# Kernel optimization log

Hardware: AMD Instinct MI355X
Metric: run time of the kernel (lower is better)

Reference implementation:

```python
import jax, jax.numpy as jnp
import numpy as np

H = 32  # rnn/encoder/residual hidden dim
NEG = -1e9


def gru(x, h0, Wih, Whh, bih, bhh):
    # x: (B,T,D), h0: (B,H); torch GRU gate order [r,z,n]
    xp = jnp.swapaxes(x @ Wih.T + bih, 0, 1)  # (T,B,3H)

    def step(h, xt):
        gh = h @ Whh.T + bhh
        xr, xz, xn = jnp.split(xt, 3, axis=-1)
        hr, hz, hn = jnp.split(gh, 3, axis=-1)
        r = jax.nn.sigmoid(xr + hr)
        z = jax.nn.sigmoid(xz + hz)
        n = jnp.tanh(xn + r * hn)
        h_new = (1.0 - z) * n + z * h
        return h_new, h_new

    hT, ys = jax.lax.scan(step, h0, xp)
    return jnp.swapaxes(ys, 0, 1), hT  # (B,T,H), (B,H)


def setup_inputs():
    key = jax.random.key(0)
    ks = jax.random.split(key, 30)
    B, T = 2048, 128
    def lin(k, o, i):
        return jax.random.normal(k, (o, i), jnp.float32) / np.sqrt(i)
    inp = {}
    inp['obs'] = jax.random.normal(ks[0], (B, T, 15), jnp.float32)
    inp['rnn_state'] = jax.random.normal(ks[1], (1, B, 3 * H), jnp.float32)
    inp['enc_air_W'] = lin(ks[2], H, 7); inp['enc_air_b'] = jnp.zeros((H,), jnp.float32)
    inp['enc_m_W'] = lin(ks[3], H, 4); inp['enc_m_b'] = jnp.zeros((H,), jnp.float32)
    inp['air_Wih'] = lin(ks[4], 3 * H, H); inp['air_Whh'] = lin(ks[5], 3 * H, H)
    inp['air_bih'] = jnp.zeros((3 * H,), jnp.float32); inp['air_bhh'] = jnp.zeros((3 * H,), jnp.float32)
    inp['m_Wih'] = lin(ks[6], 3 * H, H); inp['m_Whh'] = lin(ks[7], 3 * H, H)
    inp['m_bih'] = jnp.zeros((3 * H,), jnp.float32); inp['m_bhh'] = jnp.zeros((3 * H,), jnp.float32)
    inp['attn_in_w'] = lin(ks[8], 3 * H, H); inp['attn_in_b'] = jnp.zeros((3 * H,), jnp.float32)
    inp['attn_out_w'] = lin(ks[9], H, H); inp['attn_out_b'] = jnp.zeros((H,), jnp.float32)
    inp['mlp_W0'] = lin(ks[10], 256, 2 * H); inp['mlp_b0'] = jnp.zeros((256,), jnp.float32)
    inp['mlp_W1'] = lin(ks[11], 256, 256); inp['mlp_b1'] = jnp.zeros((256,), jnp.float32)
    inp['out_W'] = lin(ks[12], 1, 256); inp['out_b'] = jnp.zeros((1,), jnp.float32)
    return inp


def reference(obs, rnn_state, enc_air_W, enc_air_b, enc_m_W, enc_m_b,
              air_Wih, air_Whh, air_bih, air_bhh,
              m_Wih, m_Whh, m_bih, m_bhh,
              attn_in_w, attn_in_b, attn_out_w, attn_out_b,
              mlp_W0, mlp_b0, mlp_W1, mlp_b1, out_W, out_b):
    B, T, _ = obs.shape
    h_air0 = rnn_state[0, :, :H]                       # (B,H)
    h_m0 = rnn_state[0, :, H:].reshape(2 * B, H)       # faithful reshape (1,B,64)->(1,2B,32)

    # aircraft branch
    air_emb = obs[..., 8:] @ enc_air_W.T + enc_air_b   # (B,T,H)
    air_feat, next_h_air = gru(air_emb, h_air0, air_Wih, air_Whh, air_bih, air_bhh)

    # missile branch: concat missiles along batch dim
    m_raw = jnp.concatenate([obs[..., 0:4], obs[..., 4:8]], axis=0)  # (2B,T,4)
    m_emb = m_raw @ enc_m_W.T + enc_m_b
    m_feat, next_h_m = gru(m_emb, h_m0, m_Wih, m_Whh, m_bih, m_bhh)
    m1_feat, m2_feat = m_feat[:B], m_feat[B:]

    # inactive-missile mask from raw obs
    obs_flat = obs.reshape(-1, 15)
    inact = jnp.array([1.0, 0.0, 1.0, 0.0], jnp.float32)
    mask = jnp.stack([
        jnp.all(jnp.isclose(obs_flat[:, 0:4], inact), axis=-1),
        jnp.all(jnp.isclose(obs_flat[:, 4:8], inact), axis=-1),
    ], axis=1)                                          # (N,2) True = masked

    N = B * T
    air_flat = air_feat.reshape(N, H)
    m1_flat = m1_feat.reshape(N, H)
    m2_flat = m2_feat.reshape(N, H)

    # 2-head attention, q len 1, kv len 2
    Wq, Wk, Wv = jnp.split(attn_in_w, 3, axis=0)
    bq, bk, bv = jnp.split(attn_in_b, 3, axis=0)
    nh, hd = 2, H // 2
    qh = (air_flat @ Wq.T + bq).reshape(N, nh, hd)
    kv = jnp.stack([m1_flat, m2_flat], axis=1)          # (N,2,H)
    kh = (kv @ Wk.T + bk).reshape(N, 2, nh, hd)
    vh = (kv @ Wv.T + bv).reshape(N, 2, nh, hd)
    scores = jnp.einsum('nhd,nkhd->nhk', qh, kh) / np.sqrt(hd)
    scores = scores + jnp.where(mask[:, None, :], NEG, 0.0)
    w = jax.nn.softmax(scores, axis=-1)
    ctx = jnp.einsum('nhk,nkhd->nhd', w, vh).reshape(N, H)
    attn = ctx @ attn_out_w.T + attn_out_b
    attn = jnp.where(jnp.all(mask, axis=-1, keepdims=True), 0.0, attn)  # torch nan_to_num(all-masked)

    fusion = jnp.concatenate([air_flat, attn], axis=-1)  # (N,2H)
    h1 = jax.nn.leaky_relu(fusion @ mlp_W0.T + mlp_b0, 0.01)
    h2 = jax.nn.leaky_relu(h1 @ mlp_W1.T + mlp_b1, 0.01)
    val = h2 @ out_W.T + out_b                           # (N,1)

    next_h = jnp.concatenate([next_h_air, next_h_m.reshape(B, 2 * H)], axis=-1)[None]  # (1,B,96)
    return val, next_h
```

## Files before the change

### kernel.cpp

```cpp
#include <hip/hip_runtime.h>
#include <hip/hip_bf16.h>

#define BB 2048
#define TT 128
#define NN (BB*TT)
#define NVAL NN

#define OFF_BCA   768u
#define OFF_BCM   1632u
#define OFF_W0P   2048u
#define OFF_W1P   10240u
#define OFF_WQKV  43008u
#define OFF_WO    44544u
#define OFF_WH2A  45568u
#define OFF_WH2M  47104u
#define OFF_WC2A  48640u
#define OFF_WC2M  49024u
#define OFF_AIRF  83968u
#define OFF_MF    8472576u
#define OFF_MASK  25249792u

typedef __attribute__((ext_vector_type(8))) short short8;
typedef __attribute__((ext_vector_type(4))) float f32x4;
typedef _Float16 h2 __attribute__((ext_vector_type(2)));

__device__ __forceinline__ unsigned short f2bf(float f) {
    unsigned u = __builtin_bit_cast(unsigned, f);
    u += 0x7FFFu + ((u >> 16) & 1u);
    return (unsigned short)(u >> 16);
}
__device__ __forceinline__ unsigned f2h(float f) {
    _Float16 h = (_Float16)f;
    return (unsigned)__builtin_bit_cast(unsigned short, h);
}
__device__ __forceinline__ unsigned pkh2(float a, float b) {
    return (f2h(b) << 16) | f2h(a);
}
__device__ __forceinline__ float dot2(unsigned w, unsigned x, float acc) {
    return __builtin_amdgcn_fdot2(__builtin_bit_cast(h2, w),
                                  __builtin_bit_cast(h2, x), acc, false);
}

__global__ __launch_bounds__(256) void prep_kernel(
    const float* __restrict__ enc_air_W, const float* __restrict__ enc_air_b,
    const float* __restrict__ enc_m_W,   const float* __restrict__ enc_m_b,
    const float* __restrict__ air_Wih,   const float* __restrict__ air_bih,
    const float* __restrict__ m_Wih,     const float* __restrict__ m_bih,
    const float* __restrict__ air_Whh,   const float* __restrict__ m_Whh,
    const float* __restrict__ W0,        const float* __restrict__ W1,
    const float* __restrict__ attn_in_w, const float* __restrict__ attn_out_w,
    float* __restrict__ ws)
{
    int b = blockIdx.x, t = threadIdx.x;
    if (b == 0) {
        if (t < 96) {
            float bacc = air_bih[t];
            for (int k = 0; k < 32; k++) bacc += air_Wih[t*32+k] * enc_air_b[k];
            ws[OFF_BCA + t] = bacc;
            float bacc2 = m_bih[t];
            for (int k = 0; k < 32; k++) bacc2 += m_Wih[t*32+k] * enc_m_b[k];
            ws[OFF_BCM + t] = bacc2;
        }
    } else if (b <= 32) {
        unsigned short* w1p = (unsigned short*)(ws + OFF_W1P);
        int base = ((b-1)*256 + t);
        int lane = base & 63;
        int ctf  = base >> 6;
        int ct   = ctf & 15, s = ctf >> 4;
        int col = lane & 15, quad = lane >> 4;
        int k0 = s*32 + quad*8;
        int o  = ct*16 + col;
        #pragma unroll
        for (int j = 0; j < 8; j++)
            w1p[base*8 + j] = f2bf(W1[o*256 + k0 + j]);
    } else if (b <= 40) {
        unsigned short* w0p = (unsigned short*)(ws + OFF_W0P);
        int base = ((b-33)*256 + t);
        int lane = base & 63;
        int ctf  = base >> 6;
        int ct   = ctf & 15, s = ctf >> 4;
        int col = lane & 15, quad = lane >> 4;
        int k0 = s*32 + quad*8;
        int o  = ct*16 + col;
        #pragma unroll
        for (int j = 0; j < 8; j++)
            w0p[base*8 + j] = f2bf(W0[o*64 + k0 + j]);
    } else if (b == 41) {
        unsigned short* wqkv = (unsigned short*)(ws + OFF_WQKV);
        unsigned short* wop  = (unsigned short*)(ws + OFF_WO);
        for (int slot = t; slot < 512; slot += 256) {
            if (slot < 384) {
                int ct = slot >> 6, lane = slot & 63;
                int col = lane & 15, quad = lane >> 4;
                int o = ct*16 + col;
                #pragma unroll
                for (int j = 0; j < 8; j++)
                    wqkv[slot*8 + j] = f2bf(attn_in_w[o*32 + quad*8 + j]);
            } else {
                int s2 = slot - 384;
                int ct = s2 >> 6, lane = s2 & 63;
                int col = lane & 15, quad = lane >> 4;
                #pragma unroll
                for (int j = 0; j < 8; j++)
                    wop[s2*8 + j] = f2bf(attn_out_w[(ct*16+col)*32 + quad*8 + j]);
            }
        }
    } else if (b == 42) {
        unsigned* wa = (unsigned*)(ws + OFF_WH2A);
        unsigned* wm = (unsigned*)(ws + OFF_WH2M);
        for (int s = t; s < 3072; s += 256) {
            int s2 = (s < 1536) ? s : s - 1536;
            const float* W = (s < 1536) ? air_Whh : m_Whh;
            unsigned* dst = (s < 1536) ? wa : wm;
            int o = s2 >> 4, j = s2 & 15;
            dst[s2] = pkh2(W[o*32 + 2*j], W[o*32 + 2*j + 1]);
        }
    } else {
        unsigned* wa = (unsigned*)(ws + OFF_WC2A);
        unsigned* wm = (unsigned*)(ws + OFF_WC2M);
        for (int s = t; s < 768; s += 256) {
            int s2 = (s < 384) ? s : s - 384;
            bool is_air = (s < 384);
            unsigned* dst = is_air ? wa : wm;
            int o = s2 >> 2, j = s2 & 3;
            int ni  = is_air ? 7 : 4;
            float c0 = 0.f, c1 = 0.f;
            int i0 = 2*j, i1 = 2*j + 1;
            if (i0 < ni)
                for (int k = 0; k < 32; k++)
                    c0 += (is_air ? air_Wih[o*32+k]*enc_air_W[k*7+i0]
                                  : m_Wih[o*32+k]*enc_m_W[k*4+i0]);
            if (i1 < ni)
                for (int k = 0; k < 32; k++)
                    c1 += (is_air ? air_Wih[o*32+k]*enc_air_W[k*7+i1]
                                  : m_Wih[o*32+k]*enc_m_W[k*4+i1]);
            dst[s2] = pkh2(c0, c1);
        }
    }
}

template<int NI, int NP, bool DO_MASK>
__device__ void gru_row(const float* __restrict__ in_base,
                        const unsigned* __restrict__ wc2,
                        const float* __restrict__ bc,
                        const unsigned* __restrict__ wh2,
                        const float* __restrict__ bhh,
                        float h0,
                        float* __restrict__ feat_out,
                        float* __restrict__ hT_out,
                        float* __restrict__ mask_out,
                        int lane, int half)
{
    unsigned whr[16], whz[16], whn[16];
    #pragma unroll
    for (int j = 0; j < 16; j++) {
        whr[j] = wh2[lane*16 + j];
        whz[j] = wh2[(32+lane)*16 + j];
        whn[j] = wh2[(64+lane)*16 + j];
    }
    unsigned cr2[NP], cz2[NP], cn2[NP];
    #pragma unroll
    for (int j = 0; j < NP; j++) {
        cr2[j] = wc2[lane*4 + j];
        cz2[j] = wc2[(32+lane)*4 + j];
        cn2[j] = wc2[(64+lane)*4 + j];
    }
    const float bcr = bc[lane], bcz = bc[32+lane], bcn = bc[64+lane];
    const float bhr = bhh[lane], bhz = bhh[32+lane], bhn = bhh[64+lane];

    float h = h0;
    for (int t = 0; t < TT; t++) {
        float xin = (lane < NI) ? in_base[t*15 + lane] : 0.f;

        bool ok = true;
        if (DO_MASK) {
            bool pred = true;
            if (lane < 4) {
                const float c   = ((lane & 1) == 0) ? 1.f : 0.f;
                const float thr = ((lane & 1) == 0) ? 1.00001e-5f : 1e-8f;
                pred = fabsf(xin - c) <= thr;
            }
            unsigned long long ball = __ballot(pred);
            ok = (((ball >> (half*32)) & 0xFull) == 0xFull);
        }

        unsigned x16 = f2h(xin);
        unsigned xnb = (unsigned)__shfl_xor((int)x16, 1, 32);
        unsigned xpk = (xnb << 16) | x16;

        float ar = bcr, az = bcz, an = bcn;
        #pragma unroll
        for (int j = 0; j < NP; j++) {
            unsigned px = (unsigned)__shfl((int)xpk, 2*j, 32);
            ar = dot2(cr2[j], px, ar);
            az = dot2(cz2[j], px, az);
            an = dot2(cn2[j], px, an);
        }

        unsigned h16 = f2h(h);
        unsigned hnb = (unsigned)__shfl_xor((int)h16, 1, 32);
        unsigned hpk = (hnb << 16) | h16;

        float hr = bhr, hz = bhz, hn = bhn;
        #pragma unroll
        for (int j = 0; j < 16; j++) {
            unsigned ph = (unsigned)__shfl((int)hpk, 2*j, 32);
            hr = dot2(whr[j], ph, hr);
            hz = dot2(whz[j], ph, hz);
            hn = dot2(whn[j], ph, hn);
        }

        float r = 1.f / (1.f + __expf(-(ar + hr)));
        float z = 1.f / (1.f + __expf(-(az + hz)));
        float pre = an + r*hn;
        float e2 = __expf(2.f*pre);
        float n = 1.f - 2.f/(e2 + 1.f);
        h = n + z*(h - n);
        feat_out[t*32 + lane] = h;
        if (DO_MASK && lane == 0) mask_out[t*2] = ok ? 1.f : 0.f;
    }
    *hT_out = h;
}

__global__ __launch_bounds__(256) void gru_kernel(
    const float* __restrict__ obs, const float* __restrict__ rnn,
    const float* __restrict__ ws,
    const float* __restrict__ air_bhh, const float* __restrict__ m_bhh,
    float* __restrict__ air_feat, float* __restrict__ m_feat,
    float* __restrict__ mask_f, float* __restrict__ nh_out)
{
    int lane = threadIdx.x & 31;
    int half = (threadIdx.x >> 5) & 1;
    int r = blockIdx.x*8 + (threadIdx.x >> 5);
    if (r < BB) {
        const float* in_base = obs + r*(TT*15) + 8;
        float h0 = rnn[r*96 + lane];
        gru_row<7,4,false>(in_base,
                         (const unsigned*)(ws + OFF_WC2A), ws + OFF_BCA,
                         (const unsigned*)(ws + OFF_WH2A), air_bhh, h0,
                         air_feat + (size_t)r*TT*32,
                         nh_out + r*96 + lane, nullptr, lane, half);
    } else {
        int i = r - BB;
        int b = (i < BB) ? i : i - BB;
        int slot = (i < BB) ? 0 : 1;
        const float* in_base = obs + b*(TT*15) + slot*4;
        float h0 = rnn[(i >> 1)*96 + 32 + (i & 1)*32 + lane];
        gru_row<4,2,true>(in_base,
                        (const unsigned*)(ws + OFF_WC2M), ws + OFF_BCM,
                        (const unsigned*)(ws + OFF_WH2M), m_bhh, h0,
                        m_feat + (size_t)i*TT*32,
                        nh_out + (i >> 1)*96 + 32 + (i & 1)*32 + lane,
                        mask_f + (size_t)(b*TT)*2 + slot, lane, half);
    }
}

__global__ __launch_bounds__(256, 4) void fused_kernel(
    const float* __restrict__ air_feat, const float* __restrict__ m_feat,
    const float* __restrict__ mask_f,
    const unsigned short* __restrict__ wqkv, const float* __restrict__ attn_in_b,
    const unsigned short* __restrict__ wop,  const float* __restrict__ attn_out_b,
    const unsigned short* __restrict__ w0p, const float* __restrict__ b0,
    const unsigned short* __restrict__ w1p, const float* __restrict__ b1,
    const float* __restrict__ outW, const float* __restrict__ outb,
    float* __restrict__ val)
{
    __shared__ unsigned short A1[64*72];
    __shared__ unsigned short U[64*136];
    __shared__ float MS[128];
    __shared__ float PS[4][64];

    unsigned short* AM  = U;
    unsigned short* CT  = U + 64*72;
    unsigned short* A2h = U;

    const int tid  = threadIdx.x;
    const int lane = tid & 63;
    const int strip = tid >> 6;
    const int col  = lane & 15;
    const int quad = lane >> 4;
    const size_t n0 = (size_t)blockIdx.x * 64;

    {
        const float4* air4 = (const float4*)air_feat;
        const float4* mf4  = (const float4*)m_feat;
        #pragma unroll
        for (int i = 0; i < 2; i++) {
            int f4 = tid + i*256;
            int row = f4 >> 3, c4 = f4 & 7;
            float4 v = air4[(n0+row)*8 + c4];
            ushort4 o; o.x=f2bf(v.x); o.y=f2bf(v.y); o.z=f2bf(v.z); o.w=f2bf(v.w);
            *(ushort4*)&A1[row*72 + c4*4] = o;
        }
        #pragma unroll
        for (int i = 0; i < 2; i++) {
            int f4 = tid + i*256;
            int row = f4 >> 3, c4 = f4 & 7;
            float4 v = mf4[(n0+row)*8 + c4];
            ushort4 o; o.x=f2bf(v.x); o.y=f2bf(v.y); o.z=f2bf(v.z); o.w=f2bf(v.w);
            *(ushort4*)&AM[row*72 + c4*4] = o;
        }
        #pragma unroll
        for (int i = 0; i < 2; i++) {
            int f4 = tid + i*256;
            int row = f4 >> 3, c4 = f4 & 7;
            float4 v = mf4[((size_t)NN + n0 + row)*8 + c4];
            ushort4 o; o.x=f2bf(v.x); o.y=f2bf(v.y); o.z=f2bf(v.z); o.w=f2bf(v.w);
            *(ushort4*)&AM[row*72 + 32 + c4*4] = o;
        }
        if (tid < 128) MS[tid] = mask_f[n0*2 + tid];
    }
    __syncthreads();

    {
        short8 a_air = *(const short8*)&A1[(strip*16 + col)*72 + quad*8];
        short8 a_m1  = *(const short8*)&AM[(strip*16 + col)*72 + quad*8];
        short8 a_m2  = *(const short8*)&AM[(strip*16 + col)*72 + 32 + quad*8];

        f32x4 q[2], k1[2], k2[2], v1[2], v2[2], ao[2];
        #pragma unroll
        for (int ct = 0; ct < 2; ct++) {
            f32x4 z = (f32x4){0.f,0.f,0.f,0.f};
            short8 wqf = *(const short8*)(wqkv + ((0+ct)*64 + lane)*8);
            short8 wkf = *(const short8*)(wqkv + ((2+ct)*64 + lane)*8);
            short8 wvf = *(const short8*)(wqkv + ((4+ct)*64 + lane)*8);
            q[ct]  = __builtin_amdgcn_mfma_f32_16x16x32_bf16(a_air, wqf, z, 0,0,0);
            k1[ct] = __builtin_amdgcn_mfma_f32_16x16x32_bf16(a_m1,  wkf, z, 0,0,0);
            k2[ct] = __builtin_amdgcn_mfma_f32_16x16x32_bf16(a_m2,  wkf, z, 0,0,0);
            v1[ct] = __builtin_amdgcn_mfma_f32_16x16x32_bf16(a_m1,  wvf, z, 0,0,0);
            v2[ct] = __builtin_amdgcn_mfma_f32_16x16x32_bf16(a_m2,  wvf, z, 0,0,0);
        }
        float bqr[2], bkr[2], bvr[2];
        #pragma unroll
        for (int ct = 0; ct < 2; ct++) {
            bqr[ct] = attn_in_b[ct*16 + col];
            bkr[ct] = attn_in_b[32 + ct*16 + col];
            bvr[ct] = attn_in_b[64 + ct*16 + col];
        }
        float p1s[2][4], p2s[2][4];
        #pragma unroll
        for (int ct = 0; ct < 2; ct++) {
            #pragma unroll
            for (int reg = 0; reg < 4; reg++) {
                float qq = q[ct][reg] + bqr[ct];
                float p1 = qq * (k1[ct][reg] + bkr[ct]);
                float p2 = qq * (k2[ct][reg] + bkr[ct]);
                #pragma unroll
                for (int m = 1; m < 16; m <<= 1) {
                    p1 += __shfl_xor(p1, m, 64);
                    p2 += __shfl_xor(p2, m, 64);
                }
                p1s[ct][reg] = p1; p2s[ct][reg] = p2;
            }
        }
        float bothm[4];
        #pragma unroll
        for (int reg = 0; reg < 4; reg++) {
            int rloc = strip*16 + quad*4 + reg;
            float m0v = MS[rloc*2], m1v = MS[rloc*2 + 1];
            bothm[reg] = (m0v > 0.5f && m1v > 0.5f) ? 1.f : 0.f;
            #pragma unroll
            for (int ct = 0; ct < 2; ct++) {
                float s1 = p1s[ct][reg]*0.25f + (m0v > 0.5f ? -1e9f : 0.f);
                float s2 = p2s[ct][reg]*0.25f + (m1v > 0.5f ? -1e9f : 0.f);
                float mx = fmaxf(s1, s2);
                float e1 = __expf(s1 - mx), e2 = __expf(s2 - mx);
                float inv = 1.f/(e1 + e2);
                float ctxv = ((v1[ct][reg] + bvr[ct])*e1 +
                              (v2[ct][reg] + bvr[ct])*e2) * inv;
                CT[rloc*40 + ct*16 + col] = f2bf(ctxv);
            }
        }
        short8 a_ctx = *(const short8*)&CT[(strip*16 + col)*40 + quad*8];
        #pragma unroll
        for (int ct = 0; ct < 2; ct++) {
            f32x4 z = (f32x4){0.f,0.f,0.f,0.f};
            short8 wof = *(const short8*)(wop + (ct*64 + lane)*8);
            ao[ct] = __builtin_amdgcn_mfma_f32_16x16x32_bf16(a_ctx, wof, z, 0,0,0);
        }
        float bor[2] = { attn_out_b[col], attn_out_b[16 + col] };
        #pragma unroll
        for (int reg = 0; reg < 4; reg++) {
            int rloc = strip*16 + quad*4 + reg;
            #pragma unroll
            for (int ct = 0; ct < 2; ct++) {
                float av = ao[ct][reg] + bor[ct];
                av = (bothm[reg] > 0.5f) ? 0.f : av;
                A1[rloc*72 + 32 + ct*16 + col] = f2bf(av);
            }
        }
    }
    __syncthreads();

    float b1r[4], owr[4];
    #pragma unroll
    for (int c = 0; c < 4; c++) {
        int ct = c*4 + strip;
        b1r[c] = b1[ct*16 + col];
        owr[c] = outW[ct*16 + col];
    }
    const float outb0 = outb[0];

    f32x4 acc2[4][4];
    #pragma unroll
    for (int s = 0; s < 4; s++)
        #pragma unroll
        for (int c = 0; c < 4; c++) acc2[s][c] = (f32x4){0.f,0.f,0.f,0.f};

    #pragma unroll
    for (int ch = 0; ch < 2; ch++) {
        f32x4 acc1[2][4];
        #pragma unroll
        for (int cl = 0; cl < 2; cl++)
            #pragma unroll
            for (int s = 0; s < 4; s++) acc1[cl][s] = (f32x4){0.f,0.f,0.f,0.f};
        #pragma unroll
        for (int ks = 0; ks < 2; ks++) {
            short8 a[4];
            #pragma unroll
            for (int s = 0; s < 4; s++)
                a[s] = *(const short8*)&A1[(s*16 + col)*72 + ks*32 + quad*8];
            #pragma unroll
            for (int cl = 0; cl < 2; cl++) {
                int ct = (ch*2 + cl)*4 + strip;
                short8 bfr = *(const short8*)(w0p + ((ks*16 + ct)*64 + lane)*8);
                #pragma unroll
                for (int s = 0; s < 4; s++)
                    acc1[cl][s] = __builtin_amdgcn_mfma_f32_16x16x32_bf16(a[s], bfr, acc1[cl][s], 0, 0, 0);
            }
        }
        if (ch == 1) __syncthreads();
        #pragma unroll
        for (int cl = 0; cl < 2; cl++) {
            int ct = (ch*2 + cl)*4 + strip;
            float b0v = b0[ct*16 + col];
            int klocal = (ct - ch*8)*16 + col;
            #pragma unroll
            for (int s = 0; s < 4; s++) {
                #pragma unroll
                for (int reg = 0; reg < 4; reg++) {
                    float h = acc1[cl][s][reg] + b0v;
                    h = (h > 0.f) ? h : 0.01f*h;
                    A2h[(s*16 + quad*4 + reg)*136 + klocal] = f2bf(h);
                }
            }
        }
        __syncthreads();
        #pragma unroll
        for (int ksl = 0; ksl < 4; ksl++) {
            int ks = ch*4 + ksl;
            short8 bfr[4];
            #pragma unroll
            for (int c = 0; c < 4; c++) {
                int ct = c*4 + strip;
                bfr[c] = *(const short8*)(w1p + ((ks*16 + ct)*64 + lane)*8);
            }
            #pragma unroll
            for (int s = 0; s < 4; s++) {
                short8 a = *(const short8*)&A2h[(s*16 + col)*136 + ksl*32 + quad*8];
                #pragma unroll
                for (int c = 0; c < 4; c++)
                    acc2[s][c] = __builtin_amdgcn_mfma_f32_16x16x32_bf16(a, bfr[c], acc2[s][c], 0, 0, 0);
            }
        }
    }

    #pragma unroll
    for (int s = 0; s < 4; s++) {
        float pv[4];
        #pragma unroll
        for (int reg = 0; reg < 4; reg++) pv[reg] = 0.f;
        #pragma unroll
        for (int c = 0; c < 4; c++) {
            #pragma unroll
            for (int reg = 0; reg < 4; reg++) {
                float h = acc2[s][c][reg] + b1r[c];
                h = (h > 0.f) ? h : 0.01f*h;
                pv[reg] += h*owr[c];
            }
        }
        #pragma unroll
        for (int reg = 0; reg < 4; reg++) {
            #pragma unroll
            for (int m = 1; m < 16; m <<= 1)
                pv[reg] += __shfl_xor(pv[reg], m, 64);
            if (col == 0) PS[strip][s*16 + quad*4 + reg] = pv[reg];
        }
    }
    __syncthreads();
    if (tid < 64)
        val[n0 + tid] = PS[0][tid] + PS[1][tid] + PS[2][tid] + PS[3][tid] + outb0;
}

extern "C" void kernel_launch(void* const* d_in, const int* in_sizes, int n_in,
                              void* d_out, int out_size, void* d_ws, size_t ws_size,
                              hipStream_t stream) {
    const float* obs        = (const float*)d_in[0];
    const float* rnn        = (const float*)d_in[1];
    const float* enc_air_W  = (const float*)d_in[2];
    const float* enc_air_b  = (const float*)d_in[3];
    const float* enc_m_W    = (const float*)d_in[4];
    const float* enc_m_b    = (const float*)d_in[5];
    const float* air_Wih    = (const float*)d_in[6];
    const float* air_Whh    = (const float*)d_in[7];
    const float* air_bih    = (const float*)d_in[8];
    const float* air_bhh    = (const float*)d_in[9];
    const float* m_Wih      = (const float*)d_in[10];
    const float* m_Whh      = (const float*)d_in[11];
    const float* m_bih      = (const float*)d_in[12];
    const float* m_bhh      = (const float*)d_in[13];
    const float* attn_in_w  = (const float*)d_in[14];
    const float* attn_in_b  = (const float*)d_in[15];
    const float* attn_out_w = (const float*)d_in[16];
    const float* attn_out_b = (const float*)d_in[17];
    const float* mlp_W0     = (const float*)d_in[18];
    const float* mlp_b0     = (const float*)d_in[19];
    const float* mlp_W1     = (const float*)d_in[20];
    const float* mlp_b1     = (const float*)d_in[21];
    const float* out_W      = (const float*)d_in[22];
    const float* out_b      = (const float*)d_in[23];

    float* ws  = (float*)d_ws;
    float* out = (float*)d_out;

    prep_kernel<<<44, 256, 0, stream>>>(enc_air_W, enc_air_b, enc_m_W, enc_m_b,
                                        air_Wih, air_bih, m_Wih, m_bih,
                                        air_Whh, m_Whh,
                                        mlp_W0, mlp_W1, attn_in_w, attn_out_w, ws);

    gru_kernel<<<768, 256, 0, stream>>>(obs, rnn, ws, air_bhh, m_bhh,
                                        ws + OFF_AIRF, ws + OFF_MF,
                                        ws + OFF_MASK, out + NVAL);

    fused_kernel<<<NN/64, 256, 0, stream>>>(ws + OFF_AIRF, ws + OFF_MF,
                                            ws + OFF_MASK,
                                            (const unsigned short*)(ws + OFF_WQKV), attn_in_b,
                                            (const unsigned short*)(ws + OFF_WO),   attn_out_b,
                                            (const unsigned short*)(ws + OFF_W0P), mlp_b0,
                                            (const unsigned short*)(ws + OFF_W1P), mlp_b1,
                                            out_W, out_b, out);
}
```

Before: 338.6 us.

## Process two GRU rows per warp and store features as bf16

Each 32-lane group now advances two independent GRU sequences in one loop, interleaving their shuffles and dot products to hide latency and halving the grid. Hidden-state features are written as bf16 directly from the GRU kernel, halving intermediate traffic and letting the fused kernel load them with plain vector copies instead of converting from fp32. The next timestep's input is prefetched one step ahead. Register pressure rises with the doubled state and there are fewer waves to hide latency with.

```diff
diff --git a/kernel.cpp b/kernel.cpp
--- a/kernel.cpp
+++ b/kernel.cpp
@@ -17,8 +17,8 @@
 #define OFF_WC2A  48640u
 #define OFF_WC2M  49024u
 #define OFF_AIRF  83968u
-#define OFF_MF    8472576u
-#define OFF_MASK  25249792u
+#define OFF_MF    4278272u
+#define OFF_MASK  12666880u
 
 typedef __attribute__((ext_vector_type(8))) short short8;
 typedef __attribute__((ext_vector_type(4))) float f32x4;
@@ -140,16 +140,17 @@
 }
 
 template<int NI, int NP, bool DO_MASK>
-__device__ void gru_row(const float* __restrict__ in_base,
-                        const unsigned* __restrict__ wc2,
-                        const float* __restrict__ bc,
-                        const unsigned* __restrict__ wh2,
-                        const float* __restrict__ bhh,
-                        float h0,
-                        float* __restrict__ feat_out,
-                        float* __restrict__ hT_out,
-                        float* __restrict__ mask_out,
-                        int lane, int half)
+__device__ void gru_pair(const float* __restrict__ inA, const float* __restrict__ inB,
+                         const unsigned* __restrict__ wc2,
+                         const float* __restrict__ bc,
+                         const unsigned* __restrict__ wh2,
+                         const float* __restrict__ bhh,
+                         float hA, float hB,
+                         unsigned short* __restrict__ featA,
+                         unsigned short* __restrict__ featB,
+                         float* __restrict__ hTA, float* __restrict__ hTB,
+                         float* __restrict__ mask_base,
+                         int lane, int half)
 {
     unsigned whr[16], whz[16], whn[16];
     #pragma unroll
@@ -168,95 +169,137 @@
     const float bcr = bc[lane], bcz = bc[32+lane], bcn = bc[64+lane];
     const float bhr = bhh[lane], bhz = bhh[32+lane], bhn = bhh[64+lane];
 
-    float h = h0;
+    float xA = (lane < NI) ? inA[lane] : 0.f;
+    float xB = (lane < NI) ? inB[lane] : 0.f;
+
     for (int t = 0; t < TT; t++) {
-        float xin = (lane < NI) ? in_base[t*15 + lane] : 0.f;
-
-        bool ok = true;
+        float nxA = 0.f, nxB = 0.f;
+        if (t < TT-1 && lane < NI) {
+            nxA = inA[(t+1)*15 + lane];
+            nxB = inB[(t+1)*15 + lane];
+        }
+
+        bool okA = true, okB = true;
         if (DO_MASK) {
-            bool pred = true;
+            bool pA = true, pB = true;
             if (lane < 4) {
                 const float c   = ((lane & 1) == 0) ? 1.f : 0.f;
                 const float thr = ((lane & 1) == 0) ? 1.00001e-5f : 1e-8f;
-                pred = fabsf(xin - c) <= thr;
-            }
-            unsigned long long ball = __ballot(pred);
-            ok = (((ball >> (half*32)) & 0xFull) == 0xFull);
-        }
-
-        unsigned x16 = f2h(xin);
-        unsigned xnb = (unsigned)__shfl_xor((int)x16, 1, 32);
-        unsigned xpk = (xnb << 16) | x16;
-
-        float ar = bcr, az = bcz, an = bcn;
+                pA = fabsf(xA - c) <= thr;
+                pB = fabsf(xB - c) <= thr;
+            }
+            unsigned long long bA = __ballot(pA);
+            unsigned long long bB = __ballot(pB);
+            okA = (((bA >> (half*32)) & 0xFull) == 0xFull);
+            okB = (((bB >> (half*32)) & 0xFull) == 0xFull);
+        }
+
+        unsigned xa16 = f2h(xA), xb16 = f2h(xB);
+        unsigned xan = (unsigned)__shfl_xor((int)xa16, 1, 32);
+        unsigned xbn = (unsigned)__shfl_xor((int)xb16, 1, 32);
+        unsigned xpkA = (xan << 16) | xa16;
+        unsigned xpkB = (xbn << 16) | xb16;
+
+        float arA = bcr, azA = bcz, anA = bcn;
+        float arB = bcr, azB = bcz, anB = bcn;
         #pragma unroll
         for (int j = 0; j < NP; j++) {
-            unsigned px = (unsigned)__shfl((int)xpk, 2*j, 32);
-            ar = dot2(cr2[j], px, ar);
-            az = dot2(cz2[j], px, az);
-            an = dot2(cn2[j], px, an);
-        }
-
-        unsigned h16 = f2h(h);
-        unsigned hnb = (unsigned)__shfl_xor((int)h16, 1, 32);
-        unsigned hpk = (hnb << 16) | h16;
-
-        float hr = bhr, hz = bhz, hn = bhn;
+            unsigned pA = (unsigned)__shfl((int)xpkA, 2*j, 32);
+            unsigned pB = (unsigned)__shfl((int)xpkB, 2*j, 32);
+            arA = dot2(cr2[j], pA, arA);  arB = dot2(cr2[j], pB, arB);
+            azA = dot2(cz2[j], pA, azA);  azB = dot2(cz2[j], pB, azB);
+            anA = dot2(cn2[j], pA, anA);  anB = dot2(cn2[j], pB, anB);
+        }
+
+        unsigned ha16 = f2h(hA), hb16 = f2h(hB);
+        unsigned han = (unsigned)__shfl_xor((int)ha16, 1, 32);
+        unsigned hbn = (unsigned)__shfl_xor((int)hb16, 1, 32);
+        unsigned hpkA = (han << 16) | ha16;
+        unsigned hpkB = (hbn << 16) | hb16;
+
+        float hrA = bhr, hzA = bhz, hnA = bhn;
+        float hrB = bhr, hzB = bhz, hnB = bhn;
         #pragma unroll
         for (int j = 0; j < 16; j++) {
-            unsigned ph = (unsigned)__shfl((int)hpk, 2*j, 32);
-            hr = dot2(whr[j], ph, hr);
-            hz = dot2(whz[j], ph, hz);
-            hn = dot2(whn[j], ph, hn);
-        }
-
-        float r = 1.f / (1.f + __expf(-(ar + hr)));
-        float z = 1.f / (1.f + __expf(-(az + hz)));
-        float pre = an + r*hn;
-        float e2 = __expf(2.f*pre);
-        float n = 1.f - 2.f/(e2 + 1.f);
-        h = n + z*(h - n);
-        feat_out[t*32 + lane] = h;
-        if (DO_MASK && lane == 0) mask_out[t*2] = ok ? 1.f : 0.f;
-    }
-    *hT_out = h;
+            unsigned pA = (unsigned)__shfl((int)hpkA, 2*j, 32);
+            unsigned pB = (unsigned)__shfl((int)hpkB, 2*j, 32);
+            hrA = dot2(whr[j], pA, hrA);  hrB = dot2(whr[j], pB, hrB);
+            hzA = dot2(whz[j], pA, hzA);  hzB = dot2(whz[j], pB, hzB);
+            hnA = dot2(whn[j], pA, hnA);  hnB = dot2(whn[j], pB, hnB);
+        }
+
+        {
+            float rA = 1.f/(1.f + __expf(-(arA + hrA)));
+            float zA = 1.f/(1.f + __expf(-(azA + hzA)));
+            float preA = anA + rA*hnA;
+            float eA = __expf(2.f*preA);
+            float nA = 1.f - 2.f/(eA + 1.f);
+            hA = nA + zA*(hA - nA);
+
+            float rB = 1.f/(1.f + __expf(-(arB + hrB)));
+            float zB = 1.f/(1.f + __expf(-(azB + hzB)));
+            float preB = anB + rB*hnB;
+            float eB = __expf(2.f*preB);
+            float nB = 1.f - 2.f/(eB + 1.f);
+            hB = nB + zB*(hB - nB);
+        }
+
+        unsigned bfA = f2bf(hA), bfB = f2bf(hB);
+        unsigned oA = (unsigned)__shfl_xor((int)bfA, 1, 32);
+        unsigned oB = (unsigned)__shfl_xor((int)bfB, 1, 32);
+        if ((lane & 1) == 0) {
+            *(unsigned*)(featA + t*32 + lane) = (oA << 16) | bfA;
+        } else {
+            *(unsigned*)(featB + t*32 + (lane-1)) = (bfB << 16) | oB;
+        }
+        if (DO_MASK && lane == 0) {
+            float2 mv; mv.x = okA ? 1.f : 0.f; mv.y = okB ? 1.f : 0.f;
+            *(float2*)(mask_base + t*2) = mv;
+        }
+        xA = nxA; xB = nxB;
+    }
+    *hTA = hA;
+    *hTB = hB;
 }
 
 __global__ __launch_bounds__(256) void gru_kernel(
     const float* __restrict__ obs, const float* __restrict__ rnn,
     const float* __restrict__ ws,
     const float* __restrict__ air_bhh, const float* __restrict__ m_bhh,
-    float* __restrict__ air_feat, float* __restrict__ m_feat,
+    unsigned short* __restrict__ air_feat, unsigned short* __restrict__ m_feat,
     float* __restrict__ mask_f, float* __restrict__ nh_out)
 {
     int lane = threadIdx.x & 31;
     int half = (threadIdx.x >> 5) & 1;
-    int r = blockIdx.x*8 + (threadIdx.x >> 5);
-    if (r < BB) {
-        const float* in_base = obs + r*(TT*15) + 8;
-        float h0 = rnn[r*96 + lane];
-        gru_row<7,4,false>(in_base,
-                         (const unsigned*)(ws + OFF_WC2A), ws + OFF_BCA,
-                         (const unsigned*)(ws + OFF_WH2A), air_bhh, h0,
-                         air_feat + (size_t)r*TT*32,
-                         nh_out + r*96 + lane, nullptr, lane, half);
+    int g = blockIdx.x*8 + (threadIdx.x >> 5);
+    if (g < 1024) {
+        int rA = g, rB = g + 1024;
+        gru_pair<7,4,false>(obs + rA*(TT*15) + 8, obs + rB*(TT*15) + 8,
+                            (const unsigned*)(ws + OFF_WC2A), ws + OFF_BCA,
+                            (const unsigned*)(ws + OFF_WH2A), air_bhh,
+                            rnn[rA*96 + lane], rnn[rB*96 + lane],
+                            air_feat + (size_t)rA*TT*32,
+                            air_feat + (size_t)rB*TT*32,
+                            nh_out + rA*96 + lane, nh_out + rB*96 + lane,
+                            nullptr, lane, half);
     } else {
-        int i = r - BB;
-        int b = (i < BB) ? i : i - BB;
-        int slot = (i < BB) ? 0 : 1;
-        const float* in_base = obs + b*(TT*15) + slot*4;
-        float h0 = rnn[(i >> 1)*96 + 32 + (i & 1)*32 + lane];
-        gru_row<4,2,true>(in_base,
-                        (const unsigned*)(ws + OFF_WC2M), ws + OFF_BCM,
-                        (const unsigned*)(ws + OFF_WH2M), m_bhh, h0,
-                        m_feat + (size_t)i*TT*32,
-                        nh_out + (i >> 1)*96 + 32 + (i & 1)*32 + lane,
-                        mask_f + (size_t)(b*TT)*2 + slot, lane, half);
+        int b = g - 1024;
+        int j = b >> 1, k = b & 1;
+        gru_pair<4,2,true>(obs + b*(TT*15), obs + b*(TT*15) + 4,
+                           (const unsigned*)(ws + OFF_WC2M), ws + OFF_BCM,
+                           (const unsigned*)(ws + OFF_WH2M), m_bhh,
+                           rnn[j*96 + 32 + k*32 + lane],
+                           rnn[(1024 + j)*96 + 32 + k*32 + lane],
+                           m_feat + (size_t)b*TT*32,
+                           m_feat + ((size_t)b + BB)*TT*32,
+                           nh_out + j*96 + 32 + k*32 + lane,
+                           nh_out + (1024 + j)*96 + 32 + k*32 + lane,
+                           mask_f + (size_t)(b*TT)*2, lane, half);
     }
 }
 
 __global__ __launch_bounds__(256, 4) void fused_kernel(
-    const float* __restrict__ air_feat, const float* __restrict__ m_feat,
+    const unsigned short* __restrict__ air_feat, const unsigned short* __restrict__ m_feat,
     const float* __restrict__ mask_f,
     const unsigned short* __restrict__ wqkv, const float* __restrict__ attn_in_b,
     const unsigned short* __restrict__ wop,  const float* __restrict__ attn_out_b,
@@ -282,32 +325,13 @@
     const size_t n0 = (size_t)blockIdx.x * 64;
 
     {
-        const float4* air4 = (const float4*)air_feat;
-        const float4* mf4  = (const float4*)m_feat;
-        #pragma unroll
-        for (int i = 0; i < 2; i++) {
-            int f4 = tid + i*256;
-            int row = f4 >> 3, c4 = f4 & 7;
-            float4 v = air4[(n0+row)*8 + c4];
-            ushort4 o; o.x=f2bf(v.x); o.y=f2bf(v.y); o.z=f2bf(v.z); o.w=f2bf(v.w);
-            *(ushort4*)&A1[row*72 + c4*4] = o;
-        }
-        #pragma unroll
-        for (int i = 0; i < 2; i++) {
-            int f4 = tid + i*256;
-            int row = f4 >> 3, c4 = f4 & 7;
-            float4 v = mf4[(n0+row)*8 + c4];
-            ushort4 o; o.x=f2bf(v.x); o.y=f2bf(v.y); o.z=f2bf(v.z); o.w=f2bf(v.w);
-            *(ushort4*)&AM[row*72 + c4*4] = o;
-        }
-        #pragma unroll
-        for (int i = 0; i < 2; i++) {
-            int f4 = tid + i*256;
-            int row = f4 >> 3, c4 = f4 & 7;
-            float4 v = mf4[((size_t)NN + n0 + row)*8 + c4];
-            ushort4 o; o.x=f2bf(v.x); o.y=f2bf(v.y); o.z=f2bf(v.z); o.w=f2bf(v.w);
-            *(ushort4*)&AM[row*72 + 32 + c4*4] = o;
-        }
+        int row = tid >> 2, c0 = (tid & 3)*8;
+        short8 va  = *(const short8*)(air_feat + (n0 + row)*32 + c0);
+        *(short8*)&A1[row*72 + c0] = va;
+        short8 vm1 = *(const short8*)(m_feat + (n0 + row)*32 + c0);
+        *(short8*)&AM[row*72 + c0] = vm1;
+        short8 vm2 = *(const short8*)(m_feat + ((size_t)NN + n0 + row)*32 + c0);
+        *(short8*)&AM[row*72 + 32 + c0] = vm2;
         if (tid < 128) MS[tid] = mask_f[n0*2 + tid];
     }
     __syncthreads();
@@ -528,11 +552,13 @@
                                         air_Whh, m_Whh,
                                         mlp_W0, mlp_W1, attn_in_w, attn_out_w, ws);
 
-    gru_kernel<<<768, 256, 0, stream>>>(obs, rnn, ws, air_bhh, m_bhh,
-                                        ws + OFF_AIRF, ws + OFF_MF,
+    gru_kernel<<<384, 256, 0, stream>>>(obs, rnn, ws, air_bhh, m_bhh,
+                                        (unsigned short*)(ws + OFF_AIRF),
+                                        (unsigned short*)(ws + OFF_MF),
                                         ws + OFF_MASK, out + NVAL);
 
-    fused_kernel<<<NN/64, 256, 0, stream>>>(ws + OFF_AIRF, ws + OFF_MF,
+    fused_kernel<<<NN/64, 256, 0, stream>>>((const unsigned short*)(ws + OFF_AIRF),
+                                            (const unsigned short*)(ws + OFF_MF),
                                             ws + OFF_MASK,
                                             (const unsigned short*)(ws + OFF_WQKV), attn_in_b,
                                             (const unsigned short*)(ws + OFF_WO),   attn_out_b,
```

New measurement: 378.8 us. 11.9% more time.
